# Performance work log

Measured on AMD Instinct MI355X. Metric: run time of the kernel, lower is better.

The kernel has to match this reference:

```python
import jax, jax.numpy as jnp
import numpy as np

# pywt db4 reconstruction low-pass (rec_lo) coefficients.
_H = np.array([
    0.23037781330885523, 0.7148465705525415, 0.6308807679295904,
    -0.02798376941698385, -0.18703481171888114, 0.030841381835986965,
    0.032883011666982945, -0.010597401784997278], dtype=np.float64)
# pywt dec_lo = _H[::-1]; conv (flipped) correlation kernel = dec_lo[::-1] = _H.
_FLO = _H
# dec_hi[k] = (-1)^(7-k) * _H[k]; correlation kernel = dec_hi[::-1] -> (-1)^k * _H[7-k].
_FHI = np.array([(-1.0) ** k * _H[7 - k] for k in range(8)])
_FILT = jnp.asarray(np.stack([_FLO, _FHI])[:, None, :], dtype=jnp.float32)  # [2,1,8]
_PAD = 7  # filter_len - 1
_LEVEL = 4


def _dwt_step(sig):
    """One pywt dwt level, mode='symmetric'. sig: [N, L] -> (cA, cD), each [N, (L+7)//2]."""
    # symmetric (half-sample) extension by filter_len-1 each side, drop first sample
    # so that stride-2 VALID correlation reproduces pywt's output phase/length.
    xp = jnp.pad(sig, ((0, 0), (_PAD, _PAD)), mode='symmetric')[:, 1:]
    out = jax.lax.conv_general_dilated(
        xp[:, None, :], _FILT, window_strides=(2,), padding='VALID',
        dimension_numbers=('NCH', 'OIH', 'NCH'))  # [N, 2, (L+7)//2]
    return out[:, 0, :], out[:, 1, :]


def setup_inputs() -> dict:
    key = jax.random.key(0)
    x = jax.random.normal(key, (64, 4096, 32), dtype=jnp.float32)  # [B, L, C]
    return {"x": x}


def reference(x):
    """Faithful batched version of pywt.wavedec(x[i,:,j], 'db4', 'symmetric', level=4).
    Returns tuple (cA4, cD4, cD3, cD2, cD1), each [B, C, scale_len]."""
    B, L, C = x.shape
    sig = jnp.transpose(x, (0, 2, 1)).reshape(B * C, L)
    details = []
    for _ in range(_LEVEL):
        sig, cd = _dwt_step(sig)
        details.append(cd)
    coeffs = [sig] + details[::-1]  # [cA_L, cD_L, ..., cD_1] like pywt.wavedec
    return tuple(c.reshape(B, C, c.shape[-1]) for c in coeffs)
```

## Files before the change

kernel.cpp:

```cpp
#include <hip/hip_runtime.h>


#define NCH 8

__device__ __forceinline__ int sym_idx(int t, int L) {
    if (t < 0) t = -1 - t;
    if (t >= L) t = 2 * L - 1 - t;
    return t;
}

__device__ __forceinline__ void level_step(
    const float* __restrict__ src, int src_base, int srcL,
    float* __restrict__ dst, int dst_base,
    int lo, int hi,
    float* __restrict__ cdRow, int ownLo, int ownHi,
    float* __restrict__ caRow,
    int c, int slot) {
    constexpr float FLO[8] = {
        0.23037781330885523f,  0.7148465705525415f,  0.6308807679295904f,
        -0.02798376941698385f, -0.18703481171888114f, 0.030841381835986965f,
        0.032883011666982945f, -0.010597401784997278f};
    constexpr float FHI[8] = {
        -0.010597401784997278f, -0.032883011666982945f, 0.030841381835986965f,
        0.18703481171888114f,  -0.02798376941698385f,  -0.6308807679295904f,
        0.7148465705525415f,   -0.23037781330885523f};

    for (int i = lo + slot; i < hi; i += 32) {
        float a = 0.f, d = 0.f;
#pragma unroll
        for (int k = 0; k < 8; ++k) {
            int t = sym_idx(2 * i - 6 + k, srcL);
            const float v = src[(t - src_base) * NCH + c];
            a = fmaf(FLO[k], v, a);
            d = fmaf(FHI[k], v, d);
        }
        if (dst) dst[(i - dst_base) * NCH + c] = a;
        if (caRow) caRow[i] = a;
        if (i >= ownLo && i < ownHi) cdRow[i] = d;
    }
}

__global__ __launch_bounds__(256) void fused_dwt_kernel(
    const float* __restrict__ x, float* __restrict__ out) {
    const int bid = blockIdx.x;
    const int work = (bid & 7) * 256 + (bid >> 3);
    const int cg = work & 3;
    const int tile = (work >> 2) & 7;
    const int b = work >> 5;

    const int tid = threadIdx.x;
    const int c = tid & 7;
    const int slot = tid >> 3;
    const int c0 = cg * 8;

    const int L0 = 4096, L1 = 2051, L2 = 1029, L3 = 518, L4 = 262;

    const int lo4 = tile * 33, hi4 = min(L4, lo4 + 33);
    const int lo3 = max(0, 2 * lo4 - 6), hi3 = min(L3, 2 * hi4);
    const int lo2 = max(0, 2 * lo3 - 6), hi2 = min(L2, 2 * hi3);
    const int lo1 = max(0, 2 * lo2 - 6), hi1 = min(L1, 2 * hi2);
    const int lox = max(0, 2 * lo1 - 6), hix = min(L0, 2 * hi1);

    __shared__ float bx[618 * NCH];
    __shared__ float b1[306 * NCH];
    __shared__ float b2[150 * NCH];
    __shared__ float b3[72 * NCH];

    const float* xb = x + (size_t)b * L0 * 32 + c0;
    const int nx = hix - lox;
    for (int q = tid; q < nx * 2; q += 256) {
        const int jj = q >> 1;
        const int h = (q & 1) * 4;
        const float4 v = *reinterpret_cast<const float4*>(xb + (size_t)(lox + jj) * 32 + h);
        *reinterpret_cast<float4*>(&bx[jj * NCH + h]) = v;
    }
    __syncthreads();

    const size_t S = 2048;
    float* outCA4 = out;
    float* outCD4 = out + S * (size_t)L4;
    float* outCD3 = out + 2 * S * (size_t)L4;
    float* outCD2 = out + 2 * S * (size_t)L4 + S * (size_t)L3;
    float* outCD1 = out + 2 * S * (size_t)L4 + S * (size_t)L3 + S * (size_t)L2;

    const size_t sig = (size_t)b * 32 + c0 + c;

    const int o1lo = tile * 264, o1hi = min(L1, o1lo + 264);
    const int o2lo = tile * 132, o2hi = min(L2, o2lo + 132);
    const int o3lo = tile * 66, o3hi = min(L3, o3lo + 66);

    level_step(bx, lox, L0, b1, lo1, lo1, hi1,
               outCD1 + sig * L1, o1lo, o1hi, nullptr, c, slot);
    __syncthreads();
    level_step(b1, lo1, L1, b2, lo2, lo2, hi2,
               outCD2 + sig * L2, o2lo, o2hi, nullptr, c, slot);
    __syncthreads();
    level_step(b2, lo2, L2, b3, lo3, lo3, hi3,
               outCD3 + sig * L3, o3lo, o3hi, nullptr, c, slot);
    __syncthreads();
    level_step(b3, lo3, L3, nullptr, 0, lo4, hi4,
               outCD4 + sig * L4, lo4, hi4, outCA4 + sig * L4, c, slot);
}

extern "C" void kernel_launch(void* const* d_in, const int* in_sizes, int n_in,
                              void* d_out, int out_size, void* d_ws, size_t ws_size,
                              hipStream_t stream) {
    const float* x = (const float*)d_in[0];
    float* out = (float*)d_out;
    fused_dwt_kernel<<<dim3(2048), dim3(256), 0, stream>>>(x, out);
}
```

Measured before the change: 32.56 us.

## Restructure fused DWT with channel-major smem, register-blocked filtering, staged coalesced stores

Reworks the fused four-level wavelet kernel. Shared memory is now laid out channel-major with pre-materialised symmetric padding, so each thread reads a contiguous float4 window and computes several outputs in registers. Detail coefficients are staged in shared memory and written to global with aligned float4 stores, replacing strided per-element global writes. Blocks now cover 4 channels instead of 8 and the grid doubles, with boundary tiles specialised by template. The cost is more complex index math, extra shared memory, extra syncs, and edge-handling code that must stay exactly right.

```diff
diff --git a/kernel.cpp b/kernel.cpp
--- a/kernel.cpp
+++ b/kernel.cpp
@@ -1,21 +1,30 @@
 #include <hip/hip_runtime.h>
 
 
-#define NCH 8
-
-__device__ __forceinline__ int sym_idx(int t, int L) {
-    if (t < 0) t = -1 - t;
-    if (t >= L) t = 2 * L - 1 - t;
-    return t;
-}
-
-__device__ __forceinline__ void level_step(
-    const float* __restrict__ src, int src_base, int srcL,
-    float* __restrict__ dst, int dst_base,
-    int lo, int hi,
-    float* __restrict__ cdRow, int ownLo, int ownHi,
-    float* __restrict__ caRow,
-    int c, int slot) {
+#define NT 256
+#define NCHB 4
+
+#define LPX 644
+#define LP1 324
+#define LP2 164
+#define LP3 84
+#define CDPA 320
+#define CDPB 164
+#define CAP4 40
+
+#define L0C 4096
+#define L1C 2051
+#define L2C 1029
+#define L3C 518
+#define L4C 262
+#define SC 2048
+
+#define OFF_CD4 (SC * L4C)
+#define OFF_CD3 (2 * SC * L4C)
+#define OFF_CD2 (OFF_CD3 + SC * L3C)
+#define OFF_CD1 (OFF_CD2 + SC * L2C)
+
+__device__ __forceinline__ void filt8(const float* w, float& a, float& d) {
     constexpr float FLO[8] = {
         0.23037781330885523f,  0.7148465705525415f,  0.6308807679295904f,
         -0.02798376941698385f, -0.18703481171888114f, 0.030841381835986965f,
@@ -24,88 +33,227 @@
         -0.010597401784997278f, -0.032883011666982945f, 0.030841381835986965f,
         0.18703481171888114f,  -0.02798376941698385f,  -0.6308807679295904f,
         0.7148465705525415f,   -0.23037781330885523f};
-
-    for (int i = lo + slot; i < hi; i += 32) {
-        float a = 0.f, d = 0.f;
-#pragma unroll
-        for (int k = 0; k < 8; ++k) {
-            int t = sym_idx(2 * i - 6 + k, srcL);
-            const float v = src[(t - src_base) * NCH + c];
-            a = fmaf(FLO[k], v, a);
-            d = fmaf(FHI[k], v, d);
-        }
-        if (dst) dst[(i - dst_base) * NCH + c] = a;
-        if (caRow) caRow[i] = a;
-        if (i >= ownLo && i < ownHi) cdRow[i] = d;
-    }
-}
-
-__global__ __launch_bounds__(256) void fused_dwt_kernel(
+    float a0 = FLO[0] * w[0];
+    a0 = fmaf(FLO[1], w[1], a0); a0 = fmaf(FLO[2], w[2], a0); a0 = fmaf(FLO[3], w[3], a0);
+    float a1 = FLO[4] * w[4];
+    a1 = fmaf(FLO[5], w[5], a1); a1 = fmaf(FLO[6], w[6], a1); a1 = fmaf(FLO[7], w[7], a1);
+    a = a0 + a1;
+    float d0 = FHI[0] * w[0];
+    d0 = fmaf(FHI[1], w[1], d0); d0 = fmaf(FHI[2], w[2], d0); d0 = fmaf(FHI[3], w[3], d0);
+    float d1 = FHI[4] * w[4];
+    d1 = fmaf(FHI[5], w[5], d1); d1 = fmaf(FHI[6], w[6], d1); d1 = fmaf(FHI[7], w[7], d1);
+    d = d0 + d1;
+}
+
+template <int R, bool MG, bool LAST>
+__device__ __forceinline__ void level_run(
+    const float* __restrict__ rowbase, int srclo, int spad,
+    float* __restrict__ drowA, int DL,
+    float* __restrict__ cdrow, float* __restrict__ carow,
+    int lo, int hi, int slot) {
+    constexpr int NW = 2 * R + 6;
+    constexpr int NQ = (NW + 3) / 4;
+    const int span = hi - lo;
+    int i0r = slot * R;
+    const int cap = (span - R) & ~1;
+    if (i0r > cap) i0r = cap;
+    const int i0 = lo + i0r;
+
+    const float4* rq = reinterpret_cast<const float4*>(rowbase + (2 * i0 - 6 - srclo + spad));
+    float w[NQ * 4];
+#pragma unroll
+    for (int j = 0; j < NQ; ++j) {
+        const float4 t4 = rq[j];
+        w[4 * j + 0] = t4.x; w[4 * j + 1] = t4.y;
+        w[4 * j + 2] = t4.z; w[4 * j + 3] = t4.w;
+    }
+    float av[R], dv[R];
+#pragma unroll
+    for (int r = 0; r < R; ++r) filt8(&w[2 * r], av[r], dv[r]);
+
+    if constexpr (!LAST) {
+        float2* dp2 = reinterpret_cast<float2*>(drowA + i0);
+#pragma unroll
+        for (int m = 0; m < R / 2; ++m) dp2[m] = make_float2(av[2 * m], av[2 * m + 1]);
+        if constexpr (MG) {
+#pragma unroll
+            for (int r = 0; r < R; ++r) {
+                const int i = i0 + r;
+                if (i < 6) drowA[-1 - i] = av[r];
+                if (i >= DL - 7) drowA[2 * DL - 1 - i] = av[r];
+            }
+        }
+    } else {
+#pragma unroll
+        for (int r = 0; r < R; ++r) carow[i0 + r] = av[r];
+    }
+#pragma unroll
+    for (int r = 0; r < R; ++r) cdrow[i0 + r] = dv[r];
+
+    if (((span - R) & 1) && slot == 0) {
+        const int i = hi - 1;
+        const float2* r2 = reinterpret_cast<const float2*>(rowbase + (2 * i - 6 - srclo + spad));
+        float ww[8];
+#pragma unroll
+        for (int j = 0; j < 4; ++j) { const float2 t2 = r2[j]; ww[2 * j] = t2.x; ww[2 * j + 1] = t2.y; }
+        float a, d;
+        filt8(ww, a, d);
+        if constexpr (!LAST) {
+            drowA[i] = a;
+            if constexpr (MG) { if (i >= DL - 7) drowA[2 * DL - 1 - i] = a; }
+        } else {
+            carow[i] = a;
+        }
+        cdrow[i] = d;
+    }
+}
+
+__device__ __forceinline__ void dump_seg(
+    const float* __restrict__ buf, int CDP, int lo, int Len,
+    float* __restrict__ gchunk, int ownLo, int ownHi, int sigB, int tid) {
+#pragma unroll
+    for (int c2 = 0; c2 < NCHB; ++c2) {
+        const int g = (sigB + c2) * Len;
+        const int padc = (g + lo) & 3;
+        const float* srow = buf + c2 * CDP + padc - lo;
+        float* grow = gchunk + g;
+        const int a0 = ownLo + ((4 - ((g + ownLo) & 3)) & 3);
+        const int a1 = ownHi - ((g + ownHi) & 3);
+        if (tid < a0 - ownLo) grow[ownLo + tid] = srow[ownLo + tid];
+        const int ntail = ownHi - a1;
+        if (tid >= 8 && tid < 8 + ntail) grow[a1 + tid - 8] = srow[a1 + tid - 8];
+        const int n4 = (a1 - a0) >> 2;
+        for (int k = tid; k < n4; k += NT) {
+            const int i = a0 + 4 * k;
+            *reinterpret_cast<float4*>(grow + i) = *reinterpret_cast<const float4*>(srow + i);
+        }
+    }
+}
+
+template <bool MG>
+__device__ __forceinline__ void run_cascade(
+    float* bx, float* b1, float* b2, float* b3,
+    float* cdA, float* cdB, float* caB,
+    float* __restrict__ out, int sigB, int tile, int c, int slot, int tid,
+    int lox, int lo1, int hi1, int lo2, int hi2, int lo3, int hi3, int lo4, int hi4) {
+    const int xpad = 6 + (lox & 3);
+    const int p1 = 6 + (lo1 & 3);
+    const int p2 = 6 + (lo2 & 3);
+    const int p3 = 6 + (lo3 & 3);
+
+    const int o1lo = tile ? 272 * tile - 34 : 0;
+    const int o1hi = (tile == 7) ? L1C : 272 * tile + 238;
+    const int o2lo = tile ? 136 * tile - 10 : 0;
+    const int o2hi = (tile == 7) ? L2C : 136 * tile + 126;
+    const int o3lo = tile ? 68 * tile - 2 : 0;
+    const int o3hi = (tile == 7) ? L3C : 68 * tile + 66;
+
+    {
+        float* drow = b1 + c * LP1 + p1 - lo1;
+        float* cdrow = cdA + c * CDPA + (((sigB + c) * L1C + lo1) & 3) - lo1;
+        level_run<6, MG, false>(bx + c * LPX, lox, xpad, drow, L1C, cdrow, nullptr, lo1, hi1, slot);
+    }
+    __syncthreads();
+
+    dump_seg(cdA, CDPA, lo1, L1C, out + OFF_CD1, o1lo, o1hi, sigB, tid);
+    {
+        float* drow = b2 + c * LP2 + p2 - lo2;
+        float* cdrow = cdB + c * CDPB + (((sigB + c) * L2C + lo2) & 3) - lo2;
+        level_run<4, MG, false>(b1 + c * LP1, lo1, p1, drow, L2C, cdrow, nullptr, lo2, hi2, slot);
+    }
+    __syncthreads();
+
+    dump_seg(cdB, CDPB, lo2, L2C, out + OFF_CD2, o2lo, o2hi, sigB, tid);
+    {
+        float* drow = b3 + c * LP3 + p3 - lo3;
+        float* cdrow = cdA + c * CDPA + (((sigB + c) * L3C + lo3) & 3) - lo3;
+        level_run<2, MG, false>(b2 + c * LP2, lo2, p2, drow, L3C, cdrow, nullptr, lo3, hi3, slot);
+    }
+    __syncthreads();
+
+    dump_seg(cdA, CDPA, lo3, L3C, out + OFF_CD3, o3lo, o3hi, sigB, tid);
+    {
+        float* cdrow = cdB + c * CDPB + (((sigB + c) * L4C + lo4) & 3) - lo4;
+        float* carow = caB + c * CAP4 + (((sigB + c) * L4C + lo4) & 3) - lo4;
+        level_run<2, MG, true>(b3 + c * LP3, lo3, p3, nullptr, L4C, cdrow, carow, lo4, hi4, slot);
+    }
+    __syncthreads();
+
+    dump_seg(cdB, CDPB, lo4, L4C, out + OFF_CD4, lo4, hi4, sigB, tid);
+    dump_seg(caB, CAP4, lo4, L4C, out, lo4, hi4, sigB, tid);
+}
+
+__global__ __launch_bounds__(NT, 5) void fused_dwt_kernel(
     const float* __restrict__ x, float* __restrict__ out) {
+    __shared__ __align__(16) float bx[NCHB * LPX];
+    __shared__ __align__(16) float b1[NCHB * LP1];
+    __shared__ __align__(16) float b2[NCHB * LP2];
+    __shared__ __align__(16) float b3[NCHB * LP3];
+    __shared__ __align__(16) float cdA[NCHB * CDPA];
+    __shared__ __align__(16) float cdB[NCHB * CDPB];
+    __shared__ __align__(16) float caB[NCHB * CAP4];
+
     const int bid = blockIdx.x;
-    const int work = (bid & 7) * 256 + (bid >> 3);
-    const int cg = work & 3;
-    const int tile = (work >> 2) & 7;
-    const int b = work >> 5;
+    const int work = (bid & 7) * 512 + (bid >> 3);
+    const int cg = work & 7;
+    const int tile = (work >> 3) & 7;
+    const int b = work >> 6;
 
     const int tid = threadIdx.x;
-    const int c = tid & 7;
-    const int slot = tid >> 3;
-    const int c0 = cg * 8;
-
-    const int L0 = 4096, L1 = 2051, L2 = 1029, L3 = 518, L4 = 262;
-
-    const int lo4 = tile * 33, hi4 = min(L4, lo4 + 33);
-    const int lo3 = max(0, 2 * lo4 - 6), hi3 = min(L3, 2 * hi4);
-    const int lo2 = max(0, 2 * lo3 - 6), hi2 = min(L2, 2 * hi3);
-    const int lo1 = max(0, 2 * lo2 - 6), hi1 = min(L1, 2 * hi2);
-    const int lox = max(0, 2 * lo1 - 6), hix = min(L0, 2 * hi1);
-
-    __shared__ float bx[618 * NCH];
-    __shared__ float b1[306 * NCH];
-    __shared__ float b2[150 * NCH];
-    __shared__ float b3[72 * NCH];
-
-    const float* xb = x + (size_t)b * L0 * 32 + c0;
-    const int nx = hix - lox;
-    for (int q = tid; q < nx * 2; q += 256) {
-        const int jj = q >> 1;
-        const int h = (q & 1) * 4;
-        const float4 v = *reinterpret_cast<const float4*>(xb + (size_t)(lox + jj) * 32 + h);
-        *reinterpret_cast<float4*>(&bx[jj * NCH + h]) = v;
-    }
-    __syncthreads();
-
-    const size_t S = 2048;
-    float* outCA4 = out;
-    float* outCD4 = out + S * (size_t)L4;
-    float* outCD3 = out + 2 * S * (size_t)L4;
-    float* outCD2 = out + 2 * S * (size_t)L4 + S * (size_t)L3;
-    float* outCD1 = out + 2 * S * (size_t)L4 + S * (size_t)L3 + S * (size_t)L2;
-
-    const size_t sig = (size_t)b * 32 + c0 + c;
-
-    const int o1lo = tile * 264, o1hi = min(L1, o1lo + 264);
-    const int o2lo = tile * 132, o2hi = min(L2, o2lo + 132);
-    const int o3lo = tile * 66, o3hi = min(L3, o3lo + 66);
-
-    level_step(bx, lox, L0, b1, lo1, lo1, hi1,
-               outCD1 + sig * L1, o1lo, o1hi, nullptr, c, slot);
-    __syncthreads();
-    level_step(b1, lo1, L1, b2, lo2, lo2, hi2,
-               outCD2 + sig * L2, o2lo, o2hi, nullptr, c, slot);
-    __syncthreads();
-    level_step(b2, lo2, L2, b3, lo3, lo3, hi3,
-               outCD3 + sig * L3, o3lo, o3hi, nullptr, c, slot);
-    __syncthreads();
-    level_step(b3, lo3, L3, nullptr, 0, lo4, hi4,
-               outCD4 + sig * L4, lo4, hi4, outCA4 + sig * L4, c, slot);
+    const int c = tid & 3;
+    const int slot = tid >> 2;
+    const int c0 = cg * 4;
+    const int sigB = b * 32 + c0;
+
+    const int lo4 = 34 * tile, hi4 = min(L4C, lo4 + 34);
+    const int lo3 = max(0, 2 * lo4 - 6), hi3 = min(L3C, 2 * hi4);
+    const int lo2 = max(0, 2 * lo3 - 6), hi2 = min(L2C, 2 * hi3);
+    const int lo1 = max(0, 2 * lo2 - 6), hi1 = min(L1C, 2 * hi2);
+    const int lox = max(0, 2 * lo1 - 6), hix = min(L0C, 2 * hi1);
+
+    const int xpad = 6 + (lox & 3);
+    const float* xb = x + (size_t)b * (L0C * 32) + c0;
+    const int npair = (hix - lox) >> 1;
+    for (int q = tid; q < npair; q += NT) {
+        const int j = q << 1;
+        const int t = lox + j;
+        const float4 va = *reinterpret_cast<const float4*>(xb + (size_t)t * 32);
+        const float4 vb = *reinterpret_cast<const float4*>(xb + (size_t)(t + 1) * 32);
+        const float avv[4] = {va.x, va.y, va.z, va.w};
+        const float bvv[4] = {vb.x, vb.y, vb.z, vb.w};
+#pragma unroll
+        for (int hh = 0; hh < 4; ++hh)
+            *reinterpret_cast<float2*>(bx + hh * LPX + xpad + j) = make_float2(avv[hh], bvv[hh]);
+        if (lox == 0 && t < 6) {
+#pragma unroll
+            for (int hh = 0; hh < 4; ++hh) {
+                bx[hh * LPX + xpad - 1 - t] = avv[hh];
+                if (t + 1 < 6) bx[hh * LPX + xpad - 2 - t] = bvv[hh];
+            }
+        }
+        if (hix == L0C && t + 1 >= L0C - 7) {
+#pragma unroll
+            for (int hh = 0; hh < 4; ++hh) {
+                if (t >= L0C - 7) bx[hh * LPX + (2 * L0C - 1 - t) - lox + xpad] = avv[hh];
+                bx[hh * LPX + (2 * L0C - 2 - t) - lox + xpad] = bvv[hh];
+            }
+        }
+    }
+    __syncthreads();
+
+    if (tile == 0 || tile == 7)
+        run_cascade<true>(bx, b1, b2, b3, cdA, cdB, caB, out, sigB, tile, c, slot, tid,
+                          lox, lo1, hi1, lo2, hi2, lo3, hi3, lo4, hi4);
+    else
+        run_cascade<false>(bx, b1, b2, b3, cdA, cdB, caB, out, sigB, tile, c, slot, tid,
+                           lox, lo1, hi1, lo2, hi2, lo3, hi3, lo4, hi4);
 }
 
 extern "C" void kernel_launch(void* const* d_in, const int* in_sizes, int n_in,
                               void* d_out, int out_size, void* d_ws, size_t ws_size,
                               hipStream_t stream) {
+    (void)in_sizes; (void)n_in; (void)d_ws; (void)ws_size; (void)out_size;
     const float* x = (const float*)d_in[0];
     float* out = (float*)d_out;
-    fused_dwt_kernel<<<dim3(2048), dim3(256), 0, stream>>>(x, out);
-}
+    fused_dwt_kernel<<<dim3(4096), dim3(NT), 0, stream>>>(x, out);
+}
```

After: 34.44 us. 1.06x slower.
